# Performance work log

Measured on AMD Instinct MI355X. Metric: run time of the kernel, lower is better.

## Reference

```python
import jax, jax.numpy as jnp
import numpy as np


def _dct_cos_matrix(n: int, dtype=jnp.float32) -> jnp.ndarray:
    # C[k, i] = cos(pi * (2i + 1) * k / (2n))  -- unnormalized DCT-II basis
    k = jnp.arange(n, dtype=dtype)[:, None]
    i = jnp.arange(n, dtype=dtype)[None, :]
    return jnp.cos((jnp.pi / (2.0 * n)) * (2.0 * i + 1.0) * k).astype(dtype)


def setup_inputs() -> dict:
    key = jax.random.key(0)
    x = jax.random.normal(key, (4096, 4096), dtype=jnp.float32)
    return {"x": x}


def reference(x) -> jnp.ndarray:
    # 2D DCT-II (separable): out[u, v] = sum_{i,j} x[i,j]
    #   * cos(pi*(2i+1)u / (2M)) * cos(pi*(2j+1)v / (2N))
    # This matches the repo's dct2 semantics (scipy dct2(norm=None)/4,
    # i.e. plain cosine sums without the factor-2 convention).
    M, N = x.shape
    C0 = _dct_cos_matrix(M, x.dtype)  # [M, M], rows indexed by output freq u
    C1 = _dct_cos_matrix(N, x.dtype)  # [N, N], rows indexed by output freq v
    # C0 @ x -> DCT along rows dim; (.) @ C1.T -> DCT along cols dim
    return jnp.einsum('ui,ij,vj->uv', C0, x, C1, optimize=True)
```

## Files before the change

kernel.cpp:

```cpp
#include <hip/hip_runtime.h>
#include <math.h>

#define NN 4096
#define NT 128

typedef __attribute__((ext_vector_type(8))) short short8;
typedef __attribute__((ext_vector_type(4))) float f32x4;
typedef unsigned int uint32;
typedef unsigned short u16;

__device__ __forceinline__ u16 f2bf(float f) {
    uint32 u = __float_as_uint(f);
    return (u16)((u + 0x7FFFu + ((u >> 16) & 1u)) >> 16);
}

__device__ __forceinline__ void gload_lds16(const u16* g, u16* l) {
    __builtin_amdgcn_global_load_lds(
        (const __attribute__((address_space(1))) uint32*)g,
        (__attribute__((address_space(3))) uint32*)l, 16, 0, 0);
}

__global__ __launch_bounds__(256) void gen_tables(u16* __restrict__ Chi) {
    const int idx = blockIdx.x * 256 + threadIdx.x;
    const int r  = idx >> 10;
    const int c4 = (idx & 1023) << 2;
    const float W  = (float)(M_PI / 8192.0);
    const float fr = (float)r;
    ushort4 hv;
    u16* hp = (u16*)&hv;
#pragma unroll
    for (int t = 0; t < 4; ++t) {
        const int c = c4 + t;
        const float wc = W * (float)(2 * c + 1);
        hp[t] = f2bf(cosf(wc * fr));
    }
    *(ushort4*)(Chi + (size_t)r * NN + c4) = hv;
}

__global__ __launch_bounds__(256) void transpose_round(const float* __restrict__ x,
                                                       u16* __restrict__ xthi) {
    __shared__ float tile[64][65];
    const int tid = threadIdx.x;
    const int r0 = blockIdx.y * 64, c0 = blockIdx.x * 64;
    const int tr = tid >> 4, tc4 = (tid & 15) * 4;
#pragma unroll
    for (int p = 0; p < 4; ++p) {
        const int row = p * 16 + tr;
        const float4 v = *(const float4*)(x + (size_t)(r0 + row) * NN + c0 + tc4);
        tile[row][tc4 + 0] = v.x;
        tile[row][tc4 + 1] = v.y;
        tile[row][tc4 + 2] = v.z;
        tile[row][tc4 + 3] = v.w;
    }
    __syncthreads();
#pragma unroll
    for (int p = 0; p < 4; ++p) {
        const int jj = p * 16 + tr;
        ushort4 hv;
        u16* hp = (u16*)&hv;
#pragma unroll
        for (int q = 0; q < 4; ++q)
            hp[q] = f2bf(tile[tc4 + q][jj]);
        *(ushort4*)(xthi + (size_t)(c0 + jj) * NN + r0 + tc4) = hv;
    }
}

template <int SPLIT>
__global__ __launch_bounds__(512, 2) void gemm_bf16(
    const u16* __restrict__ A, const u16* __restrict__ B,
    float* __restrict__ Dout, u16* __restrict__ Dhi) {
    __shared__ u16 lds[2 * 2 * 8192];
    const int tid = threadIdx.x;
    const int w = tid >> 6, l = tid & 63;
    const int wr = w >> 2, wc = w & 3;
    const int lrow = l & 15, kh = l >> 4;
    const int row0 = blockIdx.y * 256, col0 = blockIdx.x * 256;

    f32x4 acc[8][4];
#pragma unroll
    for (int i = 0; i < 8; ++i)
#pragma unroll
        for (int j = 0; j < 4; ++j)
            acc[i][j] = (f32x4){0.f, 0.f, 0.f, 0.f};

    const int v0 = tid, v1 = tid + 512;
    const int r0s = v0 >> 2, c0s = ((v0 & 3) ^ ((v0 >> 4) & 3)) * 8;
    const int r1s = v1 >> 2, c1s = ((v1 & 3) ^ ((v1 >> 4) & 3)) * 8;
    const u16* pA0 = A + (size_t)(row0 + r0s) * NN + c0s;
    const u16* pA1 = A + (size_t)(row0 + r1s) * NN + c1s;
    const u16* pB0 = B + (size_t)(col0 + r0s) * NN + c0s;
    const u16* pB1 = B + (size_t)(col0 + r1s) * NN + c1s;
    const int d0 = (0 * 512 + w * 64) * 8;
    const int d1 = (1 * 512 + w * 64) * 8;

#define STAGE(buf, koff)                                                     \
    do {                                                                     \
        u16* Lb = &lds[(buf) * 16384];                                       \
        gload_lds16(pA0 + (koff), Lb + 0 * 8192 + d0);                       \
        gload_lds16(pA1 + (koff), Lb + 0 * 8192 + d1);                       \
        gload_lds16(pB0 + (koff), Lb + 1 * 8192 + d0);                       \
        gload_lds16(pB1 + (koff), Lb + 1 * 8192 + d1);                       \
    } while (0)

    STAGE(0, 0);

    for (int t = 0; t < NT; ++t) {
        const int cur = t & 1;
        if (t + 1 < NT) {
            STAGE(cur ^ 1, (t + 1) * 32);
            asm volatile("s_waitcnt vmcnt(4)" ::: "memory");
        } else {
            asm volatile("s_waitcnt vmcnt(0)" ::: "memory");
        }
        __builtin_amdgcn_s_barrier();
        asm volatile("" ::: "memory");

        const u16* Lb = &lds[cur * 16384];
        short8 af[8], bf[4];
#pragma unroll
        for (int fm = 0; fm < 8; ++fm) {
            const int ar = wr * 128 + fm * 16 + lrow;
            af[fm] = *(const short8*)&Lb[0 * 8192 + ar * 32 + ((kh ^ ((ar >> 2) & 3)) * 8)];
        }
#pragma unroll
        for (int fn = 0; fn < 4; ++fn) {
            const int br = wc * 64 + fn * 16 + lrow;
            bf[fn] = *(const short8*)&Lb[1 * 8192 + br * 32 + ((kh ^ ((br >> 2) & 3)) * 8)];
        }
#pragma unroll
        for (int fm = 0; fm < 8; ++fm)
#pragma unroll
            for (int fn = 0; fn < 4; ++fn)
                acc[fm][fn] = __builtin_amdgcn_mfma_f32_16x16x32_bf16(
                    af[fm], bf[fn], acc[fm][fn], 0, 0, 0);
        asm volatile("s_waitcnt lgkmcnt(0)" ::: "memory");
        __builtin_amdgcn_s_barrier();
        asm volatile("" ::: "memory");
    }
#undef STAGE

#pragma unroll
    for (int fm = 0; fm < 8; ++fm) {
#pragma unroll
        for (int fn = 0; fn < 4; ++fn) {
#pragma unroll
            for (int m = 0; m < 4; ++m) {
                const int row = row0 + wr * 128 + fm * 16 + kh * 4 + m;
                const int col = col0 + wc * 64 + fn * 16 + lrow;
                const float f = acc[fm][fn][m];
                if (SPLIT) {
                    Dhi[(size_t)row * NN + col] = f2bf(f);
                } else {
                    Dout[(size_t)row * NN + col] = f;
                }
            }
        }
    }
}

extern "C" void kernel_launch(void* const* d_in, const int* in_sizes, int n_in,
                              void* d_out, int out_size, void* d_ws, size_t ws_size,
                              hipStream_t stream) {
    const float* x = (const float*)d_in[0];
    float* out = (float*)d_out;
    u16* Chi  = (u16*)d_ws;
    u16* xthi = Chi  + (size_t)NN * NN;
    u16* Thi  = xthi + (size_t)NN * NN;

    gen_tables<<<dim3((NN * (NN / 4)) / 256), 256, 0, stream>>>(Chi);
    transpose_round<<<dim3(NN / 64, NN / 64), 256, 0, stream>>>(x, xthi);

    dim3 grid(NN / 256, NN / 256);
    gemm_bf16<1><<<grid, 512, 0, stream>>>(Chi, xthi, nullptr, Thi);
    gemm_bf16<0><<<grid, 512, 0, stream>>>(Thi, Chi, out, nullptr);
}
```

Before: 375.3 us.

## Deepen GEMM K-tile to 64 with staggered A/B staging and prioritized MFMA phases

Doubles the K depth of each staged LDS tile from 32 to 64, halving the number of outer iterations, and switches to an 8-chunk XOR swizzle. A and B loads for the next tile are issued at different points in the iteration, so the B prefetch overlaps the MFMA phases. Each tile's compute is split into four quarter phases that reuse B fragments, with s_setprio raised around the MFMA bursts. LDS per block grows to 128 KB, which likely allows only one 512-thread block per CU despite launch_bounds(512,2), and the extra barriers per tile add sync overhead.

```diff
diff --git a/kernel.cpp b/kernel.cpp
--- a/kernel.cpp
+++ b/kernel.cpp
@@ -2,7 +2,7 @@
 #include <math.h>
 
 #define NN 4096
-#define NT 128
+#define NTILES 64
 
 typedef __attribute__((ext_vector_type(8))) short short8;
 typedef __attribute__((ext_vector_type(4))) float f32x4;
@@ -19,6 +19,9 @@
         (const __attribute__((address_space(1))) uint32*)g,
         (__attribute__((address_space(3))) uint32*)l, 16, 0, 0);
 }
+
+#define BAR()   do { __builtin_amdgcn_s_barrier(); asm volatile("" ::: "memory"); } while (0)
+#define LGKM0() asm volatile("s_waitcnt lgkmcnt(0)" ::: "memory")
 
 __global__ __launch_bounds__(256) void gen_tables(u16* __restrict__ Chi) {
     const int idx = blockIdx.x * 256 + threadIdx.x;
@@ -69,7 +72,7 @@
 __global__ __launch_bounds__(512, 2) void gemm_bf16(
     const u16* __restrict__ A, const u16* __restrict__ B,
     float* __restrict__ Dout, u16* __restrict__ Dhi) {
-    __shared__ u16 lds[2 * 2 * 8192];
+    __shared__ u16 lds[2 * 2 * 16384];
     const int tid = threadIdx.x;
     const int w = tid >> 6, l = tid & 63;
     const int wr = w >> 2, wc = w & 3;
@@ -83,61 +86,112 @@
         for (int j = 0; j < 4; ++j)
             acc[i][j] = (f32x4){0.f, 0.f, 0.f, 0.f};
 
-    const int v0 = tid, v1 = tid + 512;
-    const int r0s = v0 >> 2, c0s = ((v0 & 3) ^ ((v0 >> 4) & 3)) * 8;
-    const int r1s = v1 >> 2, c1s = ((v1 & 3) ^ ((v1 >> 4) & 3)) * 8;
-    const u16* pA0 = A + (size_t)(row0 + r0s) * NN + c0s;
-    const u16* pA1 = A + (size_t)(row0 + r1s) * NN + c1s;
-    const u16* pB0 = B + (size_t)(col0 + r0s) * NN + c0s;
-    const u16* pB1 = B + (size_t)(col0 + r1s) * NN + c1s;
-    const int d0 = (0 * 512 + w * 64) * 8;
-    const int d1 = (1 * 512 + w * 64) * 8;
-
-#define STAGE(buf, koff)                                                     \
+    const int rA = tid >> 3;
+    const int c8 = (((tid & 7) ^ ((tid >> 3) & 7)) * 8);
+    const u16* pA = A + (size_t)(row0 + rA) * NN + c8;
+    const u16* pB = B + (size_t)(col0 + rA) * NN + c8;
+
+#define STAGE_A(kt, buf)                                                     \
     do {                                                                     \
-        u16* Lb = &lds[(buf) * 16384];                                       \
-        gload_lds16(pA0 + (koff), Lb + 0 * 8192 + d0);                       \
-        gload_lds16(pA1 + (koff), Lb + 0 * 8192 + d1);                       \
-        gload_lds16(pB0 + (koff), Lb + 1 * 8192 + d0);                       \
-        gload_lds16(pB1 + (koff), Lb + 1 * 8192 + d1);                       \
+        u16* Ld = &lds[(buf) * 32768 + 0 * 16384 + w * 512];                 \
+        const u16* gs = pA + (size_t)(kt) * 64;                              \
+        _Pragma("unroll") for (int s = 0; s < 4; ++s)                        \
+            gload_lds16(gs + (size_t)s * 64 * NN, Ld + s * 4096);            \
     } while (0)
-
-    STAGE(0, 0);
-
-    for (int t = 0; t < NT; ++t) {
-        const int cur = t & 1;
-        if (t + 1 < NT) {
-            STAGE(cur ^ 1, (t + 1) * 32);
+#define STAGE_B(kt, buf)                                                     \
+    do {                                                                     \
+        u16* Ld = &lds[(buf) * 32768 + 1 * 16384 + w * 512];                 \
+        const u16* gs = pB + (size_t)(kt) * 64;                              \
+        _Pragma("unroll") for (int s = 0; s < 4; ++s)                        \
+            gload_lds16(gs + (size_t)s * 64 * NN, Ld + s * 4096);            \
+    } while (0)
+
+    auto rdA = [&](short8* d, const u16* L, int rbase, int ks) {
+#pragma unroll
+        for (int f = 0; f < 4; ++f) {
+            const int r = rbase + f * 16 + lrow;
+            d[f] = *(const short8*)&L[r * 64 + (((ks * 4 + kh) ^ (r & 7)) * 8)];
+        }
+    };
+    auto rdB = [&](short8* d, const u16* L, int rbase, int ks) {
+#pragma unroll
+        for (int f = 0; f < 4; ++f) {
+            const int r = rbase + f * 16 + lrow;
+            d[f] = *(const short8*)&L[r * 64 + (((ks * 4 + kh) ^ (r & 7)) * 8)];
+        }
+    };
+
+    STAGE_A(0, 0);
+    STAGE_B(0, 0);
+
+    for (int j = 0; j < NTILES; ++j) {
+        const int cur = j & 1;
+        if (j + 1 < NTILES) {
+            STAGE_A(j + 1, cur ^ 1);
             asm volatile("s_waitcnt vmcnt(4)" ::: "memory");
         } else {
             asm volatile("s_waitcnt vmcnt(0)" ::: "memory");
         }
-        __builtin_amdgcn_s_barrier();
-        asm volatile("" ::: "memory");
-
-        const u16* Lb = &lds[cur * 16384];
-        short8 af[8], bf[4];
-#pragma unroll
-        for (int fm = 0; fm < 8; ++fm) {
-            const int ar = wr * 128 + fm * 16 + lrow;
-            af[fm] = *(const short8*)&Lb[0 * 8192 + ar * 32 + ((kh ^ ((ar >> 2) & 3)) * 8)];
-        }
-#pragma unroll
-        for (int fn = 0; fn < 4; ++fn) {
-            const int br = wc * 64 + fn * 16 + lrow;
-            bf[fn] = *(const short8*)&Lb[1 * 8192 + br * 32 + ((kh ^ ((br >> 2) & 3)) * 8)];
-        }
-#pragma unroll
-        for (int fm = 0; fm < 8; ++fm)
+        BAR();
+
+        const u16* LA = &lds[cur * 32768];
+        const u16* LB = &lds[cur * 32768 + 16384];
+        short8 a[4], b[4];
+
+        rdA(a, LA, wr * 128, 0);
+        rdB(b, LB, wc * 64, 0);
+        BAR(); LGKM0();
+        __builtin_amdgcn_s_setprio(1);
+#pragma unroll
+        for (int fm = 0; fm < 4; ++fm)
 #pragma unroll
             for (int fn = 0; fn < 4; ++fn)
                 acc[fm][fn] = __builtin_amdgcn_mfma_f32_16x16x32_bf16(
-                    af[fm], bf[fn], acc[fm][fn], 0, 0, 0);
-        asm volatile("s_waitcnt lgkmcnt(0)" ::: "memory");
-        __builtin_amdgcn_s_barrier();
-        asm volatile("" ::: "memory");
-    }
-#undef STAGE
+                    a[fm], b[fn], acc[fm][fn], 0, 0, 0);
+        __builtin_amdgcn_s_setprio(0);
+        BAR();
+        if (j + 1 < NTILES) STAGE_B(j + 1, cur ^ 1);
+
+        rdA(a, LA, wr * 128 + 64, 0);
+        BAR(); LGKM0();
+        __builtin_amdgcn_s_setprio(1);
+#pragma unroll
+        for (int fm = 0; fm < 4; ++fm)
+#pragma unroll
+            for (int fn = 0; fn < 4; ++fn)
+                acc[4 + fm][fn] = __builtin_amdgcn_mfma_f32_16x16x32_bf16(
+                    a[fm], b[fn], acc[4 + fm][fn], 0, 0, 0);
+        __builtin_amdgcn_s_setprio(0);
+        BAR();
+
+        rdA(a, LA, wr * 128, 1);
+        rdB(b, LB, wc * 64, 1);
+        BAR(); LGKM0();
+        __builtin_amdgcn_s_setprio(1);
+#pragma unroll
+        for (int fm = 0; fm < 4; ++fm)
+#pragma unroll
+            for (int fn = 0; fn < 4; ++fn)
+                acc[fm][fn] = __builtin_amdgcn_mfma_f32_16x16x32_bf16(
+                    a[fm], b[fn], acc[fm][fn], 0, 0, 0);
+        __builtin_amdgcn_s_setprio(0);
+        BAR();
+
+        rdA(a, LA, wr * 128 + 64, 1);
+        BAR(); LGKM0();
+        __builtin_amdgcn_s_setprio(1);
+#pragma unroll
+        for (int fm = 0; fm < 4; ++fm)
+#pragma unroll
+            for (int fn = 0; fn < 4; ++fn)
+                acc[4 + fm][fn] = __builtin_amdgcn_mfma_f32_16x16x32_bf16(
+                    a[fm], b[fn], acc[4 + fm][fn], 0, 0, 0);
+        __builtin_amdgcn_s_setprio(0);
+        LGKM0();
+        BAR();
+    }
+#undef STAGE_A
+#undef STAGE_B
 
 #pragma unroll
     for (int fm = 0; fm < 8; ++fm) {
```

Result: no change. 370.5 us (-1.3%).
